# Kernel tuning notes

Measured on AMD Instinct MI355X. Metric: run time of the kernel, lower is better.

Reference implementation:

```python
import jax, jax.numpy as jnp
import numpy as np

B, T, C, KQ = 4096, 128, 20, 100
SCALE = 1.0 / np.sqrt(128.0)  # 1/sqrt(input_length)


def setup_inputs() -> dict:
    key = jax.random.key(0)
    ks = jax.random.split(key, 4)
    x = jax.random.normal(ks[0], (B, T, C), dtype=jnp.float32)
    Wk = jax.random.normal(ks[1], (C, KQ), dtype=jnp.float32) * (1.0 / np.sqrt(C))
    Wq = jax.random.normal(ks[2], (C, KQ), dtype=jnp.float32) * (1.0 / np.sqrt(C))
    Wv = jax.random.normal(ks[3], (C, C), dtype=jnp.float32) * (1.0 / np.sqrt(C))
    bk = jnp.zeros((KQ,), dtype=jnp.float32)
    bq = jnp.zeros((KQ,), dtype=jnp.float32)
    bv = jnp.zeros((C,), dtype=jnp.float32)
    return {"x": x, "Wk": Wk, "bk": bk, "Wq": Wq, "bq": bq, "Wv": Wv, "bv": bv}


def reference(x, Wk, bk, Wq, bq, Wv, bv):
    # Dropout layers are identity at inference.
    k = jax.nn.elu(jnp.einsum('btc,ck->btk', x, Wk) + bk)   # [B,T,KQ]
    q = jax.nn.elu(jnp.einsum('btc,ck->btk', x, Wq) + bq)   # [B,T,KQ]
    v = jnp.tanh(jnp.einsum('btc,cd->btd', x, Wv) + bv)      # [B,T,C]
    # batch_dot(k, q^T): scores[b, i, j] = sum_d k[b,i,d] * q[b,j,d]
    w = jnp.einsum('bid,bjd->bij', k, q) * SCALE              # [B,T,T]
    # Keras Softmax(axis=1): normalize over the first seq axis (rows)
    w = jax.nn.softmax(w, axis=1)
    y = jnp.einsum('bij,bjd->bid', w, v) + x                  # [B,T,C]
    return y
```

## Files before the change

### kernel.cpp

```cpp
#include <hip/hip_runtime.h>
#include <hip/hip_bf16.h>

#define T 128
#define C 20
#define KQ 100
#define NT 256
#define SCALE 0.08838834764831845f
#define K2E   0.12751744f
#define LOG2E 1.4426950408889634f
#define TWOL2E 2.885390081777927f
#define KSTR 128
#define LDS8 136

typedef float  f32x4  __attribute__((ext_vector_type(4)));
typedef short  bf16x8 __attribute__((ext_vector_type(8)));
typedef unsigned int uint32;

__device__ __forceinline__ float exp2i(float x) { return __builtin_amdgcn_exp2f(x); }
__device__ __forceinline__ float rcpi(float x)  { return __builtin_amdgcn_rcpf(x); }

__device__ __forceinline__ short f2bf(float f) {
    unsigned u = __builtin_bit_cast(unsigned, f);
    unsigned r = (u + 0x7FFFu + ((u >> 16) & 1u)) >> 16;
    return (short)r;
}
__device__ __forceinline__ uint32 pk2(float a, float b) {
    __hip_bfloat162 h = __float22bfloat162_rn(float2{a, b});
    uint32 r;
    __builtin_memcpy(&r, &h, 4);
    return r;
}
__device__ __forceinline__ int pkfp8x4(float a, float b, float c, float d) {
    int r = __builtin_amdgcn_cvt_pk_fp8_f32(a, b, 0, false);
    r = __builtin_amdgcn_cvt_pk_fp8_f32(c, d, r, true);
    return r;
}
__device__ __forceinline__ unsigned char fp8_1(float a) {
    return (unsigned char)(__builtin_amdgcn_cvt_pk_fp8_f32(a, 0.f, 0, false) & 0xff);
}

__global__ void prep(const float* __restrict__ Wk, const float* __restrict__ bk,
                     const float* __restrict__ Wq, const float* __restrict__ bq,
                     const float* __restrict__ Wv, const float* __restrict__ bv,
                     short* __restrict__ wkT, short* __restrict__ wqT,
                     short* __restrict__ wvT)
{
    const int t = blockIdx.x * blockDim.x + threadIdx.x;
    if (t < 112 * 32) {
        const int n = t >> 5, c = t & 31;
        float vk = 0.f, vq = 0.f;
        if (n < KQ) {
            if (c < C)       { vk = Wk[c * KQ + n]; vq = Wq[c * KQ + n]; }
            else if (c == C) { vk = bk[n];          vq = bq[n]; }
        }
        wkT[t] = f2bf(vk);
        wqT[t] = f2bf(vq);
        if (t < 32 * 32) {
            const int n2 = t >> 5, c2 = t & 31;
            float vv = 0.f;
            if (n2 < C) {
                if (c2 < C)       vv = Wv[c2 * C + n2] * TWOL2E;
                else if (c2 == C) vv = bv[n2] * TWOL2E;
            }
            wvT[t] = f2bf(vv);
        }
    }
}

__global__ __launch_bounds__(NT, 4) void sa_fused(
    const float* __restrict__ x,
    const short* __restrict__ wAll,
    float* __restrict__ y)
{
    __shared__ __align__(16) unsigned char kp8[T * KSTR];
    __shared__ __align__(16) unsigned char q8 [T * KSTR];
    __shared__ __align__(16) unsigned char vT8[32 * LDS8];

    const int tid  = threadIdx.x;
    const int lane = tid & 63;
    const int w    = __builtin_amdgcn_readfirstlane(tid >> 6);
    const int quad = lane >> 4;
    const int l16  = lane & 15;
    const int b    = blockIdx.x;
    const float* xb = x + (size_t)b * (T * C);

    const int sx = (l16 & 7) << 4;
    int cx[4];
    #pragma unroll
    for (int ks = 0; ks < 4; ++ks) cx[ks] = (ks * 32 + quad * 8) ^ sx;

    float4 fA[2], fB[2];
    #pragma unroll
    for (int h = 0; h < 2; ++h) {
        const float* xr = xb + ((w + 4 * h) * 16 + l16) * C;
        fA[h] = (float4){0.f, 0.f, 0.f, 0.f};
        fB[h] = (float4){0.f, 0.f, 0.f, 0.f};
        if (quad < 2) {
            fA[h] = *(const float4*)(xr + quad * 8);
            fB[h] = *(const float4*)(xr + quad * 8 + 4);
        } else if (quad == 2) {
            fA[h] = *(const float4*)(xr + 16);
        }
    }

    if (tid < T) {
        const int sp = (tid & 7) << 4;
        const uint4 z4 = {0u, 0u, 0u, 0u};
        *(uint4*)&kp8[tid * KSTR + (112 ^ sp)] = z4;
        *(uint4*)&q8 [tid * KSTR + (112 ^ sp)] = z4;
    }

    bf16x8 xf[2];
    #pragma unroll
    for (int h = 0; h < 2; ++h) {
        uint32 p0 = 0, p1 = 0, p2 = 0, p3 = 0;
        if (quad < 2) {
            p0 = pk2(fA[h].x, fA[h].y); p1 = pk2(fA[h].z, fA[h].w);
            p2 = pk2(fB[h].x, fB[h].y); p3 = pk2(fB[h].z, fB[h].w);
        } else if (quad == 2) {
            p0 = pk2(fA[h].x, fA[h].y); p1 = pk2(fA[h].z, fA[h].w);
            p2 = pk2(1.f, 0.f);
        }
        uint4 u4; u4.x = p0; u4.y = p1; u4.z = p2; u4.w = p3;
        xf[h] = __builtin_bit_cast(bf16x8, u4);
    }

    const int colq = quad * 4;
    #pragma unroll
    for (int grp = 0; grp < 4; ++grp) {
        bf16x8 wfr[4];
        #pragma unroll
        for (int t = 0; t < 4; ++t)
            wfr[t] = *(const bf16x8*)(wAll + ((grp * 4 + t) * 16 + l16) * 32 + quad * 8);
        #pragma unroll
        for (int s = 0; s < 4; ++s) {
            const int tt = grp * 4 + s;
            #pragma unroll
            for (int h = 0; h < 2; ++h) {
                const int row = (w + 4 * h) * 16 + l16;
                const f32x4 cc = __builtin_amdgcn_mfma_f32_16x16x32_bf16(
                    wfr[s], xf[h], (f32x4){0.f, 0.f, 0.f, 0.f}, 0, 0, 0);
                if (tt < 14) {
                    float e[4];
                    #pragma unroll
                    for (int r = 0; r < 4; ++r) {
                        const float z = cc[r];
                        e[r] = __builtin_amdgcn_fmed3f(z, exp2i(z * LOG2E) - 1.f, 0.f);
                    }
                    const int col = (((tt < 7 ? tt : tt - 7) * 16) ^ sx) + colq;
                    unsigned char* dst = (tt < 7)
                        ? &kp8[row * KSTR + col]
                        : &q8 [row * KSTR + col];
                    *(int*)dst = pkfp8x4(e[0], e[1], e[2], e[3]);
                } else {
                    #pragma unroll
                    for (int r = 0; r < 4; ++r) {
                        const float e2 = exp2i(cc[r]);
                        vT8[((tt - 14) * 16 + quad * 4 + r) * LDS8 + row]
                            = fp8_1(fmaf(-2.f, rcpi(e2 + 1.f), 1.f));
                    }
                }
            }
        }
    }
    __syncthreads();

    f32x4 acc[2][8];
    #pragma unroll
    for (int h = 0; h < 2; ++h)
        #pragma unroll
        for (int nt = 0; nt < 8; ++nt) acc[h][nt] = (f32x4){0.f, 0.f, 0.f, 0.f};
    __builtin_amdgcn_s_setprio(1);
    #pragma unroll
    for (int ks = 0; ks < 4; ++ks) {
        const long a0 = *(const long*)&q8[( w      * 16 + l16) * KSTR + cx[ks]];
        const long a1 = *(const long*)&q8[((w + 4) * 16 + l16) * KSTR + cx[ks]];
        #pragma unroll
        for (int nt = 0; nt < 8; ++nt) {
            const long bk8 = *(const long*)&kp8[(nt * 16 + l16) * KSTR + cx[ks]];
            acc[0][nt] = __builtin_amdgcn_mfma_f32_16x16x32_fp8_fp8(a0, bk8, acc[0][nt], 0, 0, 0);
            acc[1][nt] = __builtin_amdgcn_mfma_f32_16x16x32_fp8_fp8(a1, bk8, acc[1][nt], 0, 0, 0);
        }
    }
    __builtin_amdgcn_s_setprio(0);

    float ssum[2][4];
    #pragma unroll
    for (int h = 0; h < 2; ++h) {
        #pragma unroll
        for (int r = 0; r < 4; ++r) ssum[h][r] = 0.f;
        #pragma unroll
        for (int nt = 0; nt < 8; ++nt)
            #pragma unroll
            for (int r = 0; r < 4; ++r) {
                const float e = exp2i(acc[h][nt][r] * K2E);
                acc[h][nt][r] = e;
                ssum[h][r] += e;
            }
        #pragma unroll
        for (int r = 0; r < 4; ++r) {
            float s = ssum[h][r];
            s += __shfl_xor(s, 1); s += __shfl_xor(s, 2);
            s += __shfl_xor(s, 4); s += __shfl_xor(s, 8);
            ssum[h][r] = 64.f * rcpi(s);
        }
    }
    __syncthreads();

    const int pw0 = (( w      * 16 + colq) ^ sx);
    const int pw1 = (((w + 4) * 16 + colq) ^ sx);
    #pragma unroll
    for (int nt = 0; nt < 8; ++nt) {
        *(int*)&kp8[(nt * 16 + l16) * KSTR + pw0]
            = pkfp8x4(acc[0][nt][0] * ssum[0][0], acc[0][nt][1] * ssum[0][1],
                      acc[0][nt][2] * ssum[0][2], acc[0][nt][3] * ssum[0][3]);
        *(int*)&kp8[(nt * 16 + l16) * KSTR + pw1]
            = pkfp8x4(acc[1][nt][0] * ssum[1][0], acc[1][nt][1] * ssum[1][1],
                      acc[1][nt][2] * ssum[1][2], acc[1][nt][3] * ssum[1][3]);
    }
    __syncthreads();

    f32x4 yacc[2][2];
    #pragma unroll
    for (int h = 0; h < 2; ++h) {
        yacc[h][0] = (f32x4){0.f, 0.f, 0.f, 0.f};
        yacc[h][1] = (f32x4){0.f, 0.f, 0.f, 0.f};
    }
    __builtin_amdgcn_s_setprio(1);
    #pragma unroll
    for (int ks = 0; ks < 4; ++ks) {
        const long a0 = *(const long*)&kp8[( w      * 16 + l16) * KSTR + cx[ks]];
        const long a1 = *(const long*)&kp8[((w + 4) * 16 + l16) * KSTR + cx[ks]];
        #pragma unroll
        for (int nt = 0; nt < 2; ++nt) {
            const long bv8 = *(const long*)&vT8[(nt * 16 + l16) * LDS8 + ks * 32 + quad * 8];
            yacc[0][nt] = __builtin_amdgcn_mfma_f32_16x16x32_fp8_fp8(a0, bv8, yacc[0][nt], 0, 0, 0);
            yacc[1][nt] = __builtin_amdgcn_mfma_f32_16x16x32_fp8_fp8(a1, bv8, yacc[1][nt], 0, 0, 0);
        }
    }
    __builtin_amdgcn_s_setprio(0);

    {
        float* yb = y + (size_t)b * (T * C);
        const float inv64 = 1.f / 64.f;
        #pragma unroll
        for (int h = 0; h < 2; ++h)
            #pragma unroll
            for (int r = 0; r < 4; ++r) {
                const int row  = (w + 4 * h) * 16 + quad * 4 + r;
                const int base = row * C;
                yb[base + l16] = yacc[h][0][r] * inv64 + xb[base + l16];
                if (l16 < 4)
                    yb[base + 16 + l16] = yacc[h][1][r] * inv64 + xb[base + 16 + l16];
            }
    }
}

extern "C" void kernel_launch(void* const* d_in, const int* in_sizes, int n_in,
                              void* d_out, int out_size, void* d_ws, size_t ws_size,
                              hipStream_t stream) {
    const float* x  = (const float*)d_in[0];
    const float* Wk = (const float*)d_in[1];
    const float* bk = (const float*)d_in[2];
    const float* Wq = (const float*)d_in[3];
    const float* bq = (const float*)d_in[4];
    const float* Wv = (const float*)d_in[5];
    const float* bv = (const float*)d_in[6];
    float* y = (float*)d_out;

    char* ws = (char*)d_ws;
    short* wkT = (short*)ws;
    short* wqT = (short*)(ws + 7168);
    short* wvT = (short*)(ws + 14336);

    prep<<<14, 256, 0, stream>>>(Wk, bk, Wq, bq, Wv, bv, wkT, wqT, wvT);

    const int B = in_sizes[0] / (T * C);
    sa_fused<<<B, NT, 0, stream>>>(x, (const short*)ws, y);
}
```

Measured before the change: 144.0 us.

## Shrink LDS row stride to 104 and raise occupancy to five blocks

Cuts the k/q fp8 LDS row stride from 128 to 104 bytes, removes the XOR swizzle, and drops the zero-padding stores. The last K-step of the score GEMM is now a special case that masks out all lanes except quad 0. The probability matrix is split across the kp8 and q8 buffers, with columns 0-63 in one and 64-127 in the other, so it fits the narrower stride. The smaller LDS footprint lets launch bounds go from 4 to 5 blocks per CU for more occupancy, at the risk of LDS bank conflicts without the swizzle and tighter register limits.

```diff
diff --git a/kernel.cpp b/kernel.cpp
--- a/kernel.cpp
+++ b/kernel.cpp
@@ -9,7 +9,7 @@
 #define K2E   0.12751744f
 #define LOG2E 1.4426950408889634f
 #define TWOL2E 2.885390081777927f
-#define KSTR 128
+#define KSTR 104
 #define LDS8 136
 
 typedef float  f32x4  __attribute__((ext_vector_type(4)));
@@ -67,7 +67,7 @@
     }
 }
 
-__global__ __launch_bounds__(NT, 4) void sa_fused(
+__global__ __launch_bounds__(NT, 5) void sa_fused(
     const float* __restrict__ x,
     const short* __restrict__ wAll,
     float* __restrict__ y)
@@ -83,11 +83,6 @@
     const int l16  = lane & 15;
     const int b    = blockIdx.x;
     const float* xb = x + (size_t)b * (T * C);
-
-    const int sx = (l16 & 7) << 4;
-    int cx[4];
-    #pragma unroll
-    for (int ks = 0; ks < 4; ++ks) cx[ks] = (ks * 32 + quad * 8) ^ sx;
 
     float4 fA[2], fB[2];
     #pragma unroll
@@ -103,13 +98,6 @@
         }
     }
 
-    if (tid < T) {
-        const int sp = (tid & 7) << 4;
-        const uint4 z4 = {0u, 0u, 0u, 0u};
-        *(uint4*)&kp8[tid * KSTR + (112 ^ sp)] = z4;
-        *(uint4*)&q8 [tid * KSTR + (112 ^ sp)] = z4;
-    }
-
     bf16x8 xf[2];
     #pragma unroll
     for (int h = 0; h < 2; ++h) {
@@ -125,7 +113,6 @@
         xf[h] = __builtin_bit_cast(bf16x8, u4);
     }
 
-    const int colq = quad * 4;
     #pragma unroll
     for (int grp = 0; grp < 4; ++grp) {
         bf16x8 wfr[4];
@@ -147,11 +134,14 @@
                         const float z = cc[r];
                         e[r] = __builtin_amdgcn_fmed3f(z, exp2i(z * LOG2E) - 1.f, 0.f);
                     }
-                    const int col = (((tt < 7 ? tt : tt - 7) * 16) ^ sx) + colq;
-                    unsigned char* dst = (tt < 7)
-                        ? &kp8[row * KSTR + col]
-                        : &q8 [row * KSTR + col];
-                    *(int*)dst = pkfp8x4(e[0], e[1], e[2], e[3]);
+                    const int ct = (tt < 7 ? tt : tt - 7);
+                    if (ct < 6 || quad < 2) {
+                        const int col = ct * 16 + quad * 4;
+                        unsigned char* dst = (tt < 7)
+                            ? &kp8[row * KSTR + col]
+                            : &q8 [row * KSTR + col];
+                        *(int*)dst = pkfp8x4(e[0], e[1], e[2], e[3]);
+                    }
                 } else {
                     #pragma unroll
                     for (int r = 0; r < 4; ++r) {
@@ -172,12 +162,24 @@
         for (int nt = 0; nt < 8; ++nt) acc[h][nt] = (f32x4){0.f, 0.f, 0.f, 0.f};
     __builtin_amdgcn_s_setprio(1);
     #pragma unroll
-    for (int ks = 0; ks < 4; ++ks) {
-        const long a0 = *(const long*)&q8[( w      * 16 + l16) * KSTR + cx[ks]];
-        const long a1 = *(const long*)&q8[((w + 4) * 16 + l16) * KSTR + cx[ks]];
+    for (int ks = 0; ks < 3; ++ks) {
+        const long a0 = *(const long*)&q8[( w      * 16 + l16) * KSTR + ks * 32 + quad * 8];
+        const long a1 = *(const long*)&q8[((w + 4) * 16 + l16) * KSTR + ks * 32 + quad * 8];
         #pragma unroll
         for (int nt = 0; nt < 8; ++nt) {
-            const long bk8 = *(const long*)&kp8[(nt * 16 + l16) * KSTR + cx[ks]];
+            const long bk8 = *(const long*)&kp8[(nt * 16 + l16) * KSTR + ks * 32 + quad * 8];
+            acc[0][nt] = __builtin_amdgcn_mfma_f32_16x16x32_fp8_fp8(a0, bk8, acc[0][nt], 0, 0, 0);
+            acc[1][nt] = __builtin_amdgcn_mfma_f32_16x16x32_fp8_fp8(a1, bk8, acc[1][nt], 0, 0, 0);
+        }
+    }
+    {
+        const bool q0 = (quad == 0);
+        const int tof = q0 ? 96 : 0;
+        long a0 = *(const long*)&q8[( w      * 16 + l16) * KSTR + tof]; if (!q0) a0 = 0;
+        long a1 = *(const long*)&q8[((w + 4) * 16 + l16) * KSTR + tof]; if (!q0) a1 = 0;
+        #pragma unroll
+        for (int nt = 0; nt < 8; ++nt) {
+            long bk8 = *(const long*)&kp8[(nt * 16 + l16) * KSTR + tof]; if (!q0) bk8 = 0;
             acc[0][nt] = __builtin_amdgcn_mfma_f32_16x16x32_fp8_fp8(a0, bk8, acc[0][nt], 0, 0, 0);
             acc[1][nt] = __builtin_amdgcn_mfma_f32_16x16x32_fp8_fp8(a1, bk8, acc[1][nt], 0, 0, 0);
         }
@@ -207,14 +209,13 @@
     }
     __syncthreads();
 
-    const int pw0 = (( w      * 16 + colq) ^ sx);
-    const int pw1 = (((w + 4) * 16 + colq) ^ sx);
+    const int pcol = w * 16 + quad * 4;
     #pragma unroll
     for (int nt = 0; nt < 8; ++nt) {
-        *(int*)&kp8[(nt * 16 + l16) * KSTR + pw0]
+        *(int*)&kp8[(nt * 16 + l16) * KSTR + pcol]
             = pkfp8x4(acc[0][nt][0] * ssum[0][0], acc[0][nt][1] * ssum[0][1],
                       acc[0][nt][2] * ssum[0][2], acc[0][nt][3] * ssum[0][3]);
-        *(int*)&kp8[(nt * 16 + l16) * KSTR + pw1]
+        *(int*)&q8 [(nt * 16 + l16) * KSTR + pcol]
             = pkfp8x4(acc[1][nt][0] * ssum[1][0], acc[1][nt][1] * ssum[1][1],
                       acc[1][nt][2] * ssum[1][2], acc[1][nt][3] * ssum[1][3]);
     }
@@ -229,8 +230,10 @@
     __builtin_amdgcn_s_setprio(1);
     #pragma unroll
     for (int ks = 0; ks < 4; ++ks) {
-        const long a0 = *(const long*)&kp8[( w      * 16 + l16) * KSTR + cx[ks]];
-        const long a1 = *(const long*)&kp8[((w + 4) * 16 + l16) * KSTR + cx[ks]];
+        const unsigned char* pbuf = (ks < 2) ? kp8 : q8;
+        const int jcol = (ks & 1) * 32 + quad * 8;
+        const long a0 = *(const long*)&pbuf[( w      * 16 + l16) * KSTR + jcol];
+        const long a1 = *(const long*)&pbuf[((w + 4) * 16 + l16) * KSTR + jcol];
         #pragma unroll
         for (int nt = 0; nt < 2; ++nt) {
             const long bv8 = *(const long*)&vT8[(nt * 16 + l16) * LDS8 + ks * 32 + quad * 8];
```

Result: slower. 164.0 us (+13.9%).
